# Kernel optimization log

Measured on AMD Instinct MI355X. Metric: run time of the kernel, lower is better.

Reference implementation:

```python
import jax, jax.numpy as jnp
import numpy as np
import math

B, T_FUT, T_LOOK, D, H = 8, 512, 2048, 1024, 16
HD = D // H


def setup_inputs() -> dict:
    key = jax.random.key(0)
    ks = jax.random.split(key, 12)
    xav = 1.0 / math.sqrt(D)  # approx xavier_uniform scale for square [D,D]
    return {
        "encoded_representation": jax.random.normal(ks[0], (B, T_LOOK, D), jnp.float32),
        "future_queries": jax.random.normal(ks[1], (B, T_FUT, D), jnp.float32),
        "decoder_lengths": jax.random.randint(ks[2], (B,), 1, T_FUT + 1),
        "encoder_lengths": jax.random.randint(ks[3], (B,), 1, T_LOOK + 1),
        "wq_w": jax.random.normal(ks[4], (D, D), jnp.float32) * xav,
        "wq_b": jnp.zeros((D,), jnp.float32),
        "wk_w": jax.random.normal(ks[5], (D, D), jnp.float32) * xav,
        "wk_b": jnp.zeros((D,), jnp.float32),
        "wv_w": jax.random.normal(ks[6], (D, D), jnp.float32) * xav,
        "wv_b": jnp.zeros((D,), jnp.float32),
        "wo_w": jax.random.normal(ks[7], (D, D), jnp.float32) * xav,
        "wo_b": jnp.zeros((D,), jnp.float32),
    }


def reference(encoded_representation, future_queries, decoder_lengths, encoder_lengths,
              wq_w, wq_b, wk_w, wk_b, wv_w, wv_b, wo_w, wo_b):
    # variable-length padding mask: [B, 1, T_fut, T_look]
    dec_valid = jnp.arange(T_FUT)[None, :] < decoder_lengths[:, None]   # [B, T_fut]
    enc_valid = jnp.arange(T_LOOK)[None, :] < encoder_lengths[:, None]  # [B, T_look]
    mask = dec_valid[:, None, :, None] & enc_valid[:, None, None, :]

    # torch nn.Linear: y = x @ W^T + b
    Q = (future_queries @ wq_w.T + wq_b).reshape(B, T_FUT, H, HD)
    K = (encoded_representation @ wk_w.T + wk_b).reshape(B, T_LOOK, H, HD)
    V = (encoded_representation @ wv_w.T + wv_b).reshape(B, T_LOOK, H, HD)

    scores = jnp.einsum("bqhd,bkhd->bhqk", Q, K) / math.sqrt(HD)
    # NOTE: faithful to source, which fills masked positions with -1e-09 (not -1e9)
    scores = jnp.where(mask, scores, jnp.float32(-1e-09))
    probs = jax.nn.softmax(scores, axis=-1)

    attended = jnp.einsum("bhqk,bkhd->bqhd", probs, V).reshape(B, T_FUT, D)
    return attended @ wo_w.T + wo_b
```

## Files before the change

kernel.cpp:

```cpp
#include <hip/hip_runtime.h>

typedef __attribute__((ext_vector_type(4))) float f32x4;
typedef __attribute__((ext_vector_type(8))) short s16x8;

__device__ __forceinline__ ushort f2bf(float f) {
  unsigned u = __float_as_uint(f);
  return (ushort)((u + 0x7fffu + ((u >> 16) & 1u)) >> 16);
}

__global__ __launch_bounds__(256) void cvt_bf16(const float4* __restrict__ in,
                                                ushort* __restrict__ out, int n4) {
  int stride = gridDim.x * blockDim.x;
  for (int i = blockIdx.x * blockDim.x + threadIdx.x; i < n4; i += stride) {
    float4 v = in[i];
    uint2 o;
    o.x = (unsigned)f2bf(v.x) | ((unsigned)f2bf(v.y) << 16);
    o.y = (unsigned)f2bf(v.z) | ((unsigned)f2bf(v.w) << 16);
    *(uint2*)(out + (size_t)i * 4) = o;
  }
}

__global__ __launch_bounds__(256) void cvt_bf16_w4(const float4* __restrict__ a,
                                                   const float4* __restrict__ b,
                                                   const float4* __restrict__ c,
                                                   const float4* __restrict__ d,
                                                   ushort* __restrict__ oa, ushort* __restrict__ ob,
                                                   ushort* __restrict__ oc, ushort* __restrict__ od) {
  int idx = blockIdx.x * 256 + threadIdx.x;
  int sel = idx >> 18, k = idx & 262143;
  const float4* src = sel == 0 ? a : sel == 1 ? b : sel == 2 ? c : d;
  ushort* dst = sel == 0 ? oa : sel == 1 ? ob : sel == 2 ? oc : od;
  float4 v = src[k];
  uint2 o;
  o.x = (unsigned)f2bf(v.x) | ((unsigned)f2bf(v.y) << 16);
  o.y = (unsigned)f2bf(v.z) | ((unsigned)f2bf(v.w) << 16);
  *(uint2*)(dst + (size_t)k * 4) = o;
}

__device__ __forceinline__ void gload_lds16(const void* g, void* l) {
  __builtin_amdgcn_global_load_lds((const __attribute__((address_space(1))) void*)g,
                                   (__attribute__((address_space(3))) void*)l, 16, 0, 0);
}

__global__ __launch_bounds__(512, 1) void gemm256_fused(
    const ushort* __restrict__ enc16, const ushort* __restrict__ fq16,
    const ushort* __restrict__ Bkv, const ushort* __restrict__ Bq,
    const float* __restrict__ wk_b, const float* __restrict__ wv_b,
    const float* __restrict__ wq_b,
    ushort* __restrict__ Ko, ushort* __restrict__ Vt, ushort* __restrict__ Qo,
    float* __restrict__ Tsum, const int* __restrict__ dlen,
    const int* __restrict__ elen, float qscale) {
  __shared__ char lds[131072];
  const int tid = threadIdx.x;
  const int lane = tid & 63, wid = tid >> 6;
  const int g = lane >> 4, r = lane & 15;
  const int wm = wid >> 2, wn = wid & 3;
  const int bid = blockIdx.x;

  const ushort* Amat;
  const ushort* Bmat;
  int m0, n0, role;
  if (bid < 512) {
    const int xcd = bid & 7, inner = bid >> 3;
    m0 = (xcd * 8 + (inner & 7)) * 256;
    n0 = (inner >> 3) * 256;
    Amat = enc16;
    Bmat = Bkv;
    if (n0 < 1024) {
      role = 0;
      if ((m0 & 2047) >= elen[m0 >> 11]) return;
    } else {
      role = 1;
    }
  } else {
    const int q = bid - 512;
    m0 = (q & 15) * 256;
    n0 = (q >> 4) * 256;
    Amat = fq16;
    Bmat = Bq;
    role = 2;
    if ((m0 & 511) >= dlen[m0 >> 9]) return;
  }
  const size_t rowb = 2048;

  const int srow = tid >> 3;
  const int scb = (((tid & 7) ^ (srow & 7)) << 4);
  const char* Asrc = (const char*)Amat + (size_t)(m0 + srow) * rowb + scb;
  const char* Bsrc = (const char*)Bmat + (size_t)(n0 + srow) * rowb + scb;

  auto sAh = [&](int kt, int h) {
    char* d0 = lds + (kt & 1) * 32768 + h * 16384 + tid * 16;
    const char* s0 = Asrc + (size_t)(h * 128) * rowb + (size_t)kt * 128;
    gload_lds16(s0, d0);
    gload_lds16(s0 + (size_t)64 * rowb, d0 + 8192);
  };
  auto sBh = [&](int kt, int h) {
    char* d0 = lds + 65536 + (kt & 1) * 32768 + h * 16384 + tid * 16;
    const char* s0 = Bsrc + (size_t)(h * 128) * rowb + (size_t)kt * 128;
    gload_lds16(s0, d0);
    gload_lds16(s0 + (size_t)64 * rowb, d0 + 8192);
  };

  const int cb0 = (g * 16) ^ ((r & 7) << 4);
  const int cb1 = (64 + g * 16) ^ ((r & 7) << 4);

  f32x4 acc[8][4] = {};

  sAh(0, 0); sAh(0, 1); sBh(0, 0); sBh(0, 1); sBh(1, 0); sBh(1, 1);
  asm volatile("s_waitcnt vmcnt(4)" ::: "memory");
  __builtin_amdgcn_s_barrier();

#define MFMA_(a, b, c) __builtin_amdgcn_mfma_f32_16x16x32_bf16(a, b, c, 0, 0, 0)
#define PH(AB, Q, STAGE, WAIT)                                                 \
  {                                                                            \
    s16x8 aq0 = *(const s16x8*)(AB + (2 * (Q)) * 2048 + cb0);                  \
    s16x8 aq1 = *(const s16x8*)(AB + (2 * (Q)) * 2048 + cb1);                  \
    s16x8 aq2 = *(const s16x8*)(AB + (2 * (Q) + 1) * 2048 + cb0);              \
    s16x8 aq3 = *(const s16x8*)(AB + (2 * (Q) + 1) * 2048 + cb1);              \
    STAGE;                                                                     \
    __builtin_amdgcn_s_barrier();                                              \
    asm volatile("s_waitcnt lgkmcnt(0)" ::: "memory");                         \
    __builtin_amdgcn_sched_barrier(0);                                         \
    __builtin_amdgcn_s_setprio(1);                                             \
    _Pragma("unroll") for (int ni = 0; ni < 4; ++ni)                           \
        acc[2 * (Q)][ni] = MFMA_(aq0, bfr[ni][0], acc[2 * (Q)][ni]);           \
    _Pragma("unroll") for (int ni = 0; ni < 4; ++ni)                           \
        acc[2 * (Q) + 1][ni] = MFMA_(aq2, bfr[ni][0], acc[2 * (Q) + 1][ni]);   \
    _Pragma("unroll") for (int ni = 0; ni < 4; ++ni)                           \
        acc[2 * (Q)][ni] = MFMA_(aq1, bfr[ni][1], acc[2 * (Q)][ni]);           \
    _Pragma("unroll") for (int ni = 0; ni < 4; ++ni)                           \
        acc[2 * (Q) + 1][ni] = MFMA_(aq3, bfr[ni][1], acc[2 * (Q) + 1][ni]);   \
    __builtin_amdgcn_s_setprio(0);                                             \
    WAIT;                                                                      \
    __builtin_amdgcn_s_barrier();                                              \
  }
#define LOADB(BB)                                                              \
  _Pragma("unroll") for (int ni = 0; ni < 4; ++ni) {                           \
    bfr[ni][0] = *(const s16x8*)(BB + ni * 2048 + cb0);                        \
    bfr[ni][1] = *(const s16x8*)(BB + ni * 2048 + cb1);                        \
  }

  const int NIT = 8;
  const char* AbB = lds + wm * 16384 + r * 128;
  const char* BbB = lds + 65536 + (wn >> 1) * 16384 + (wn & 1) * 8192 + r * 128;

  for (int it = 0; it < NIT; ++it) {
    const bool st = (it + 1 < NIT);
    const int k1 = 2 * it + 1, k2 = 2 * it + 2, k3 = 2 * it + 3;
    s16x8 bfr[4][2];
    LOADB(BbB);
    PH(AbB, 0, sAh(k1, 0), );
    PH(AbB, 1, sAh(k1, 1), );
    PH(AbB, 2, if (st) sBh(k2, 0), );
    PH(AbB, 3, if (st) sBh(k2, 1),
       if (st) { asm volatile("s_waitcnt vmcnt(4)" ::: "memory"); } else {
         asm volatile("s_waitcnt vmcnt(0)" ::: "memory");
       });
    const char* Ab1 = AbB + 32768;
    const char* Bb1 = BbB + 32768;
    LOADB(Bb1);
    PH(Ab1, 0, if (st) sAh(k2, 0), );
    PH(Ab1, 1, if (st) sAh(k2, 1), );
    PH(Ab1, 2, if (st) sBh(k3, 0), );
    PH(Ab1, 3, if (st) sBh(k3, 1),
       if (st) { asm volatile("s_waitcnt vmcnt(4)" ::: "memory"); });
  }
#undef PH
#undef LOADB
#undef MFMA_

  if (role != 1) {
    ushort* C = (role == 2) ? Qo : Ko;
    const float* bias0 = (role == 2) ? wq_b : wk_b;
    const float sc = (role == 2) ? qscale : 1.0f;
#pragma unroll
    for (int ni = 0; ni < 4; ++ni) {
      const int col = wn * 64 + ni * 16 + r;
      const float bv = bias0[n0 + col];
#pragma unroll
      for (int i = 0; i < 8; ++i)
#pragma unroll
        for (int j = 0; j < 4; ++j) {
          const int row = wm * 128 + i * 16 + g * 4 + j;
          *(ushort*)(lds + ((row * 512 + col * 2) ^ (((row >> 2) & 7) << 4))) =
              f2bf((acc[i][ni][j] + bv) * sc);
        }
    }
    __syncthreads();
    const int c = tid & 31, r0 = tid >> 5;
#pragma unroll
    for (int u = 0; u < 16; ++u) {
      const int row = u * 16 + r0;
      s16x8 v = *(const s16x8*)(lds + ((row * 512 + c * 16) ^ (((row >> 2) & 7) << 4)));
      *(s16x8*)(C + (size_t)(m0 + row) * 1024 + n0 + c * 8) = v;
    }
  } else {
    const int nv0 = n0 - 1024;
    const int bb = m0 >> 11, tt0 = m0 & 2047;
#pragma unroll
    for (int ni = 0; ni < 4; ++ni) {
      const int nv = nv0 + wn * 64 + ni * 16 + r;
      const float bv = wv_b[nv];
#pragma unroll
      for (int qq = 0; qq < 2; ++qq) {
        float s = 0.0f;
#pragma unroll
        for (int ii = 0; ii < 4; ++ii)
#pragma unroll
          for (int j = 0; j < 4; ++j) s += acc[qq * 4 + ii][ni][j];
        s += __shfl_xor(s, 16);
        s += __shfl_xor(s, 32);
        if (g == 0) {
          const int gt = (m0 + (wm * 2 + qq) * 64) >> 6;
          Tsum[((size_t)((gt >> 5) * 16 + (nv >> 6)) * 33 + (gt & 31)) * 64 + (nv & 63)] =
              s + 64.0f * bv;
        }
      }
    }
#pragma unroll
    for (int ni = 0; ni < 4; ++ni) {
      const int rowl = wn * 64 + ni * 16 + r;
      const float bv = wv_b[nv0 + rowl];
#pragma unroll
      for (int i = 0; i < 8; ++i)
#pragma unroll
        for (int j = 0; j < 4; ++j) {
          const int coll = wm * 128 + i * 16 + g * 4 + j;
          *(ushort*)(lds + ((rowl * 512 + coll * 2) ^ ((rowl & 7) << 4))) =
              f2bf(acc[i][ni][j] + bv);
        }
    }
    __syncthreads();
    const int c = tid & 31, r0 = tid >> 5;
#pragma unroll
    for (int u = 0; u < 16; ++u) {
      const int row = u * 16 + r0;
      s16x8 v = *(const s16x8*)(lds + ((row * 512 + c * 16) ^ ((row & 7) << 4)));
      *(s16x8*)(Vt + ((size_t)bb * 1024 + nv0 + row) * 2048 + tt0 + c * 8) = v;
    }
  }
}

template <int EPI>
__global__ __launch_bounds__(256) void gemm_bt(const ushort* __restrict__ A,
                                               const ushort* __restrict__ B,
                                               const float* __restrict__ bias,
                                               void* __restrict__ Cout, float oscale,
                                               int M, int N, int K) {
  __shared__ ushort As[128 * 32];
  __shared__ ushort Bs[128 * 32];
  const int tid = threadIdx.x;
  const int lane = tid & 63, w = tid >> 6;
  const int g = lane >> 4, r = lane & 15;
  const int m0 = blockIdx.x * 128, n0 = blockIdx.y * 128;
  const int wm = (w >> 1) * 64, wn = (w & 1) * 64;

  const int srow = tid >> 2;
  const int scb = (tid & 3) * 16;
  const char* Ag = (const char*)(A + (size_t)(m0 + srow) * K) + scb;
  const char* Bg = (const char*)(B + (size_t)(n0 + srow) * K) + scb;
  char* AsB = (char*)As + (tid & 192) * 16;
  char* BsB = (char*)Bs + (tid & 192) * 16;
  const size_t rowskip = (size_t)64 * K * sizeof(ushort);

  f32x4 acc[4][4] = {};

  for (int k0 = 0; k0 < K; k0 += 32) {
    gload_lds16(Ag + (size_t)k0 * 2, AsB);
    gload_lds16(Ag + rowskip + (size_t)k0 * 2, AsB + 4096);
    gload_lds16(Bg + (size_t)k0 * 2, BsB);
    gload_lds16(Bg + rowskip + (size_t)k0 * 2, BsB + 4096);
    __syncthreads();
    s16x8 af[4], bf[4];
#pragma unroll
    for (int i = 0; i < 4; ++i) af[i] = *(const s16x8*)&As[(wm + i * 16 + r) * 32 + g * 8];
#pragma unroll
    for (int i = 0; i < 4; ++i) bf[i] = *(const s16x8*)&Bs[(wn + i * 16 + r) * 32 + g * 8];
#pragma unroll
    for (int mi = 0; mi < 4; ++mi)
#pragma unroll
      for (int ni = 0; ni < 4; ++ni)
        acc[mi][ni] =
            __builtin_amdgcn_mfma_f32_16x16x32_bf16(af[mi], bf[ni], acc[mi][ni], 0, 0, 0);
    __syncthreads();
  }

  if constexpr (EPI == 0) {
    ushort* C = (ushort*)Cout;
#pragma unroll
    for (int ni = 0; ni < 4; ++ni) {
      const int n = n0 + wn + ni * 16 + r;
      const float bv = bias[n];
#pragma unroll
      for (int mi = 0; mi < 4; ++mi) {
        const int mb = m0 + wm + mi * 16 + g * 4;
#pragma unroll
        for (int j = 0; j < 4; ++j)
          C[(size_t)(mb + j) * N + n] = f2bf((acc[mi][ni][j] + bv) * oscale);
      }
    }
  } else {
    float* C = (float*)Cout;
#pragma unroll
    for (int ni = 0; ni < 4; ++ni) {
      const int n = n0 + wn + ni * 16 + r;
      const float bv = bias[n];
#pragma unroll
      for (int mi = 0; mi < 4; ++mi) {
        const int mb = m0 + wm + mi * 16 + g * 4;
#pragma unroll
        for (int j = 0; j < 4; ++j)
          C[(size_t)(mb + j) * N + n] = acc[mi][ni][j] + bv;
      }
    }
  }
}

__global__ __launch_bounds__(64) void vsuffix(float* __restrict__ T) {
  const int bh = blockIdx.x;
  const int d = threadIdx.x;
  float* p = T + (size_t)bh * 33 * 64 + d;
  float run = 0.0f;
  p[32 * 64] = 0.0f;
  for (int t = 31; t >= 0; --t) {
    run += p[t * 64];
    p[t * 64] = run;
  }
}

__device__ __forceinline__ ushort* swz(ushort* base, int row, int colb) {
  return (ushort*)((char*)base + row * 128 + (colb ^ ((row & 7) << 4)));
}

__global__ __launch_bounds__(256) void attn_fwd(
    const ushort* __restrict__ Q, const ushort* __restrict__ Km,
    const ushort* __restrict__ Vt, const float* __restrict__ Vsuf,
    const int* __restrict__ dlen, const int* __restrict__ elen,
    ushort* __restrict__ Oatt) {
  const int tid = threadIdx.x;
  const int lane = tid & 63, w = tid >> 6;
  const int g = lane >> 4, r = lane & 15;
  const int qt = blockIdx.x, b = blockIdx.y, h = blockIdx.z;
  const int dl = dlen[b], el = elen[b];
  const float* VS = Vsuf + (size_t)(b * 16 + h) * 33 * 64;

  if (qt * 64 >= dl) {
    const int qrow = qt * 64 + w * 16 + g * 4;
#pragma unroll
    for (int dt = 0; dt < 4; ++dt) {
      const ushort hv = f2bf(VS[dt * 16 + r] * (1.0f / 2048.0f));
#pragma unroll
      for (int j = 0; j < 4; ++j)
        Oatt[(size_t)(b * 512 + qrow + j) * 1024 + h * 64 + dt * 16 + r] = hv;
    }
    return;
  }

  __shared__ ushort Ks[64 * 64];
  __shared__ ushort Vs[64 * 64];
  __shared__ ushort Ps[4 * 16 * 64];
  ushort* PsW = Ps + w * 16 * 64;
  const int qbase = qt * 64 + w * 16;

  s16x8 qf[2];
  {
    const ushort* qp = Q + (size_t)(b * 512 + qbase + r) * 1024 + h * 64 + g * 8;
    qf[0] = *(const s16x8*)qp;
    qf[1] = *(const s16x8*)(qp + 32);
  }

  f32x4 o[4] = {};
  float lrow[4] = {0.0f, 0.0f, 0.0f, 0.0f};
  bool qok[4];
#pragma unroll
  for (int j = 0; j < 4; ++j) qok[j] = (qbase + g * 4 + j) < dl;

  const int sr = tid >> 3;
  const int sc8 = (tid & 7) * 8;
  const int scb = sc8 * 2;
  const ushort* Kg = Km + (size_t)(b * 2048 + sr) * 1024 + h * 64 + sc8;
  const ushort* Vg = Vt + ((size_t)b * 1024 + h * 64 + sr) * 2048 + sc8;

  const int t_last = (el - 1) >> 6;

  s16x8 pk0, pk1, pv0, pv1;
  {
    pk0 = *(const s16x8*)(Kg);
    pk1 = *(const s16x8*)(Kg + (size_t)32 * 1024);
    pv0 = *(const s16x8*)(Vg);
    pv1 = *(const s16x8*)(Vg + (size_t)32 * 2048);
  }

  for (int t = 0; t <= t_last; ++t) {
    *(s16x8*)swz(Ks, sr, scb) = pk0;
    *(s16x8*)swz(Ks, sr + 32, scb) = pk1;
    *(s16x8*)swz(Vs, sr, scb) = pv0;
    *(s16x8*)swz(Vs, sr + 32, scb) = pv1;
    __syncthreads();

    if (t < t_last) {
      const int kv0 = (t + 1) * 64;
      pk0 = *(const s16x8*)(Kg + (size_t)kv0 * 1024);
      pk1 = *(const s16x8*)(Kg + (size_t)(kv0 + 32) * 1024);
      pv0 = *(const s16x8*)(Vg + kv0);
      pv1 = *(const s16x8*)(Vg + (size_t)32 * 2048 + kv0);
    }

    const int kv0 = t * 64;
    float p[4][4];
#pragma unroll
    for (int nt = 0; nt < 4; ++nt) {
      f32x4 s = {};
      s16x8 kf0 = *(const s16x8*)swz(Ks, nt * 16 + r, g * 16);
      s16x8 kf1 = *(const s16x8*)swz(Ks, nt * 16 + r, 64 + g * 16);
      s = __builtin_amdgcn_mfma_f32_16x16x32_bf16(qf[0], kf0, s, 0, 0, 0);
      s = __builtin_amdgcn_mfma_f32_16x16x32_bf16(qf[1], kf1, s, 0, 0, 0);
      const bool kok = (kv0 + nt * 16 + r) < el;
#pragma unroll
      for (int j = 0; j < 4; ++j) {
        const float pe = __builtin_amdgcn_exp2f(s[j]);
        p[nt][j] = (kok && qok[j]) ? pe : 1.0f;
      }
    }
#pragma unroll
    for (int nt = 0; nt < 4; ++nt)
#pragma unroll
      for (int j = 0; j < 4; ++j) lrow[j] += p[nt][j];

#pragma unroll
    for (int nt = 0; nt < 4; ++nt) {
#pragma unroll
      for (int jp = 0; jp < 4; jp += 2) {
        unsigned pk;
        asm("v_cvt_pk_bf16_f32 %0, %1, %2" : "=v"(pk) : "v"(p[nt][jp]), "v"(p[nt][jp + 1]));
        *swz(PsW, g * 4 + jp, (nt * 16 + r) * 2) = (ushort)pk;
        *swz(PsW, g * 4 + jp + 1, (nt * 16 + r) * 2) = (ushort)(pk >> 16);
      }
    }

#pragma unroll
    for (int kc = 0; kc < 2; ++kc) {
      s16x8 pf = *(const s16x8*)swz(PsW, r, kc * 64 + g * 16);
#pragma unroll
      for (int dt = 0; dt < 4; ++dt) {
        s16x8 vf = *(const s16x8*)swz(Vs, dt * 16 + r, kc * 64 + g * 16);
        o[dt] = __builtin_amdgcn_mfma_f32_16x16x32_bf16(pf, vf, o[dt], 0, 0, 0);
      }
    }
    __syncthreads();
  }

  const float tailcnt = (float)(2048 - (t_last + 1) * 64);
  const float* VT = VS + (t_last + 1) * 64;
#pragma unroll
  for (int dt = 0; dt < 4; ++dt) {
    const float tv = VT[dt * 16 + r];
#pragma unroll
    for (int j = 0; j < 4; ++j) o[dt][j] += tv;
  }

  float inv[4];
#pragma unroll
  for (int j = 0; j < 4; ++j) {
    float s = lrow[j];
    s += __shfl_xor(s, 1);
    s += __shfl_xor(s, 2);
    s += __shfl_xor(s, 4);
    s += __shfl_xor(s, 8);
    inv[j] = 1.0f / (s + tailcnt);
  }
#pragma unroll
  for (int dt = 0; dt < 4; ++dt)
#pragma unroll
    for (int j = 0; j < 4; ++j)
      Oatt[(size_t)(b * 512 + qbase + g * 4 + j) * 1024 + h * 64 + dt * 16 + r] =
          f2bf(o[dt][j] * inv[j]);
}

extern "C" void kernel_launch(void* const* d_in, const int* in_sizes, int n_in,
                              void* d_out, int out_size, void* d_ws, size_t ws_size,
                              hipStream_t stream) {
  const float* enc  = (const float*)d_in[0];
  const float* fq   = (const float*)d_in[1];
  const int* dlen   = (const int*)d_in[2];
  const int* elen   = (const int*)d_in[3];
  const float* wq_w = (const float*)d_in[4];
  const float* wq_b = (const float*)d_in[5];
  const float* wk_w = (const float*)d_in[6];
  const float* wk_b = (const float*)d_in[7];
  const float* wv_w = (const float*)d_in[8];
  const float* wv_b = (const float*)d_in[9];
  const float* wo_w = (const float*)d_in[10];
  const float* wo_b = (const float*)d_in[11];

  char* ws = (char*)d_ws;
  ushort* enc16 = (ushort*)(ws + 0);
  ushort* fq16  = (ushort*)(ws + 33554432);
  float*  Vsuf  = (float*)(ws + 41943040 + 2097152 * 4);
  ushort* wq16  = (ushort*)(ws + 41943040);
  ushort* wk16  = (ushort*)(ws + 44040192);
  ushort* wv16  = (ushort*)(ws + 46137344);
  ushort* wo16  = (ushort*)(ws + 48234496);
  ushort* Qw    = (ushort*)(ws + 52428800);
  ushort* Kw    = (ushort*)(ws + 60817408);
  ushort* Vtw   = (ushort*)(ws + 94371840);
  ushort* attw  = (ushort*)(ws + 127926272);

  cvt_bf16<<<2048, 256, 0, stream>>>((const float4*)enc, enc16, 16384 * 1024 / 4);
  cvt_bf16<<<1024, 256, 0, stream>>>((const float4*)fq, fq16, 4096 * 1024 / 4);
  cvt_bf16_w4<<<4096, 256, 0, stream>>>((const float4*)wq_w, (const float4*)wk_w,
                                        (const float4*)wv_w, (const float4*)wo_w,
                                        wq16, wk16, wv16, wo16);

  const float qscale = 0.125f * 1.44269504088896340736f;
  gemm256_fused<<<576, 512, 0, stream>>>(enc16, fq16, wk16, wq16, wk_b, wv_b, wq_b,
                                         Kw, Vtw, Qw, Vsuf, dlen, elen, qscale);
  vsuffix<<<128, 64, 0, stream>>>(Vsuf);

  attn_fwd<<<dim3(8, 8, 16), 256, 0, stream>>>(Qw, Kw, Vtw, Vsuf, dlen, elen, attw);

  gemm_bt<2><<<dim3(32, 8), 256, 0, stream>>>(attw, wo16, wo_b, d_out, 1.0f, 4096, 1024, 1024);
}
```

Measured before the change: 198.2 us.

## Make projection GEMM persistent with atomic tile queue and merge conversion kernels

The fused QKV projection GEMM now launches 256 persistent blocks. Each block pulls 256x256 tiles from a global atomic counter, and tiles masked out by the length checks are skipped without occupying a block slot. This is meant to balance load across CUs and avoid the tail effect of a 576-block grid. The three bf16 conversion kernels are merged into one grid-stride kernel, and the attention output buffer now reuses the fq16 workspace region. The changes add a memset launch and an atomic per tile, and drop the XCD-aware tile ordering. There is also a possible race on the shared tile index when a block skips a tile.

Result: slower. 319.1 us (+61.0%).

```diff
diff --git a/kernel.cpp b/kernel.cpp
--- a/kernel.cpp
+++ b/kernel.cpp
@@ -8,33 +8,34 @@
   return (ushort)((u + 0x7fffu + ((u >> 16) & 1u)) >> 16);
 }
 
-__global__ __launch_bounds__(256) void cvt_bf16(const float4* __restrict__ in,
-                                                ushort* __restrict__ out, int n4) {
-  int stride = gridDim.x * blockDim.x;
-  for (int i = blockIdx.x * blockDim.x + threadIdx.x; i < n4; i += stride) {
-    float4 v = in[i];
+__global__ __launch_bounds__(256) void cvt_all(
+    const float4* __restrict__ enc, const float4* __restrict__ fq,
+    const float4* __restrict__ wq, const float4* __restrict__ wk,
+    const float4* __restrict__ wv, const float4* __restrict__ wo,
+    ushort* __restrict__ enc16, ushort* __restrict__ fq16,
+    ushort* __restrict__ wq16, ushort* __restrict__ wk16,
+    ushort* __restrict__ wv16, ushort* __restrict__ wo16) {
+  const int stride = gridDim.x * 256;
+  for (int i = blockIdx.x * 256 + threadIdx.x; i < 6291456; i += stride) {
+    const float4* src;
+    ushort* dst;
+    int k;
+    if (i < 4194304) {
+      src = enc; dst = enc16; k = i;
+    } else if (i < 5242880) {
+      src = fq; dst = fq16; k = i - 4194304;
+    } else {
+      const int j = i - 5242880, sel = j >> 18;
+      k = j & 262143;
+      src = sel == 0 ? wq : sel == 1 ? wk : sel == 2 ? wv : wo;
+      dst = sel == 0 ? wq16 : sel == 1 ? wk16 : sel == 2 ? wv16 : wo16;
+    }
+    float4 v = src[k];
     uint2 o;
     o.x = (unsigned)f2bf(v.x) | ((unsigned)f2bf(v.y) << 16);
     o.y = (unsigned)f2bf(v.z) | ((unsigned)f2bf(v.w) << 16);
-    *(uint2*)(out + (size_t)i * 4) = o;
-  }
-}
-
-__global__ __launch_bounds__(256) void cvt_bf16_w4(const float4* __restrict__ a,
-                                                   const float4* __restrict__ b,
-                                                   const float4* __restrict__ c,
-                                                   const float4* __restrict__ d,
-                                                   ushort* __restrict__ oa, ushort* __restrict__ ob,
-                                                   ushort* __restrict__ oc, ushort* __restrict__ od) {
-  int idx = blockIdx.x * 256 + threadIdx.x;
-  int sel = idx >> 18, k = idx & 262143;
-  const float4* src = sel == 0 ? a : sel == 1 ? b : sel == 2 ? c : d;
-  ushort* dst = sel == 0 ? oa : sel == 1 ? ob : sel == 2 ? oc : od;
-  float4 v = src[k];
-  uint2 o;
-  o.x = (unsigned)f2bf(v.x) | ((unsigned)f2bf(v.y) << 16);
-  o.y = (unsigned)f2bf(v.z) | ((unsigned)f2bf(v.w) << 16);
-  *(uint2*)(dst + (size_t)k * 4) = o;
+    *(uint2*)(dst + (size_t)k * 4) = o;
+  }
 }
 
 __device__ __forceinline__ void gload_lds16(const void* g, void* l) {
@@ -49,66 +50,71 @@
     const float* __restrict__ wq_b,
     ushort* __restrict__ Ko, ushort* __restrict__ Vt, ushort* __restrict__ Qo,
     float* __restrict__ Tsum, const int* __restrict__ dlen,
-    const int* __restrict__ elen, float qscale) {
+    const int* __restrict__ elen, unsigned* __restrict__ ctr, float qscale) {
   __shared__ char lds[131072];
+  __shared__ int s_tile;
   const int tid = threadIdx.x;
   const int lane = tid & 63, wid = tid >> 6;
   const int g = lane >> 4, r = lane & 15;
   const int wm = wid >> 2, wn = wid & 3;
-  const int bid = blockIdx.x;
-
-  const ushort* Amat;
-  const ushort* Bmat;
-  int m0, n0, role;
-  if (bid < 512) {
-    const int xcd = bid & 7, inner = bid >> 3;
-    m0 = (xcd * 8 + (inner & 7)) * 256;
-    n0 = (inner >> 3) * 256;
-    Amat = enc16;
-    Bmat = Bkv;
-    if (n0 < 1024) {
-      role = 0;
-      if ((m0 & 2047) >= elen[m0 >> 11]) return;
+
+  for (;;) {
+    if (tid == 0) s_tile = (int)atomicAdd(ctr, 1u);
+    __syncthreads();
+    const int t = s_tile;
+    if (t >= 576) return;
+
+    const ushort* Amat;
+    const ushort* Bmat;
+    int m0, n0, role;
+    if (t < 512) {
+      m0 = (t & 63) * 256;
+      n0 = (t >> 6) * 256;
+      Amat = enc16;
+      Bmat = Bkv;
+      if (n0 < 1024) {
+        role = 0;
+        if ((m0 & 2047) >= elen[m0 >> 11]) continue;
+      } else {
+        role = 1;
+      }
     } else {
-      role = 1;
-    }
-  } else {
-    const int q = bid - 512;
-    m0 = (q & 15) * 256;
-    n0 = (q >> 4) * 256;
-    Amat = fq16;
-    Bmat = Bq;
-    role = 2;
-    if ((m0 & 511) >= dlen[m0 >> 9]) return;
-  }
-  const size_t rowb = 2048;
-
-  const int srow = tid >> 3;
-  const int scb = (((tid & 7) ^ (srow & 7)) << 4);
-  const char* Asrc = (const char*)Amat + (size_t)(m0 + srow) * rowb + scb;
-  const char* Bsrc = (const char*)Bmat + (size_t)(n0 + srow) * rowb + scb;
-
-  auto sAh = [&](int kt, int h) {
-    char* d0 = lds + (kt & 1) * 32768 + h * 16384 + tid * 16;
-    const char* s0 = Asrc + (size_t)(h * 128) * rowb + (size_t)kt * 128;
-    gload_lds16(s0, d0);
-    gload_lds16(s0 + (size_t)64 * rowb, d0 + 8192);
-  };
-  auto sBh = [&](int kt, int h) {
-    char* d0 = lds + 65536 + (kt & 1) * 32768 + h * 16384 + tid * 16;
-    const char* s0 = Bsrc + (size_t)(h * 128) * rowb + (size_t)kt * 128;
-    gload_lds16(s0, d0);
-    gload_lds16(s0 + (size_t)64 * rowb, d0 + 8192);
-  };
-
-  const int cb0 = (g * 16) ^ ((r & 7) << 4);
-  const int cb1 = (64 + g * 16) ^ ((r & 7) << 4);
-
-  f32x4 acc[8][4] = {};
-
-  sAh(0, 0); sAh(0, 1); sBh(0, 0); sBh(0, 1); sBh(1, 0); sBh(1, 1);
-  asm volatile("s_waitcnt vmcnt(4)" ::: "memory");
-  __builtin_amdgcn_s_barrier();
+      const int q = t - 512;
+      m0 = (q & 15) * 256;
+      n0 = (q >> 4) * 256;
+      Amat = fq16;
+      Bmat = Bq;
+      role = 2;
+      if ((m0 & 511) >= dlen[m0 >> 9]) continue;
+    }
+    const size_t rowb = 2048;
+
+    const int srow = tid >> 3;
+    const int scb = (((tid & 7) ^ (srow & 7)) << 4);
+    const char* Asrc = (const char*)Amat + (size_t)(m0 + srow) * rowb + scb;
+    const char* Bsrc = (const char*)Bmat + (size_t)(n0 + srow) * rowb + scb;
+
+    auto sAh = [&](int kt, int h) {
+      char* d0 = lds + (kt & 1) * 32768 + h * 16384 + tid * 16;
+      const char* s0 = Asrc + (size_t)(h * 128) * rowb + (size_t)kt * 128;
+      gload_lds16(s0, d0);
+      gload_lds16(s0 + (size_t)64 * rowb, d0 + 8192);
+    };
+    auto sBh = [&](int kt, int h) {
+      char* d0 = lds + 65536 + (kt & 1) * 32768 + h * 16384 + tid * 16;
+      const char* s0 = Bsrc + (size_t)(h * 128) * rowb + (size_t)kt * 128;
+      gload_lds16(s0, d0);
+      gload_lds16(s0 + (size_t)64 * rowb, d0 + 8192);
+    };
+
+    const int cb0 = (g * 16) ^ ((r & 7) << 4);
+    const int cb1 = (64 + g * 16) ^ ((r & 7) << 4);
+
+    f32x4 acc[8][4] = {};
+
+    sAh(0, 0); sAh(0, 1); sBh(0, 0); sBh(0, 1); sBh(1, 0); sBh(1, 1);
+    asm volatile("s_waitcnt vmcnt(4)" ::: "memory");
+    __builtin_amdgcn_s_barrier();
 
 #define MFMA_(a, b, c) __builtin_amdgcn_mfma_f32_16x16x32_bf16(a, b, c, 0, 0, 0)
 #define PH(AB, Q, STAGE, WAIT)                                                 \
@@ -140,113 +146,111 @@
     bfr[ni][1] = *(const s16x8*)(BB + ni * 2048 + cb1);                        \
   }
 
-  const int NIT = 8;
-  const char* AbB = lds + wm * 16384 + r * 128;
-  const char* BbB = lds + 65536 + (wn >> 1) * 16384 + (wn & 1) * 8192 + r * 128;
-
-  for (int it = 0; it < NIT; ++it) {
-    const bool st = (it + 1 < NIT);
-    const int k1 = 2 * it + 1, k2 = 2 * it + 2, k3 = 2 * it + 3;
-    s16x8 bfr[4][2];
-    LOADB(BbB);
-    PH(AbB, 0, sAh(k1, 0), );
-    PH(AbB, 1, sAh(k1, 1), );
-    PH(AbB, 2, if (st) sBh(k2, 0), );
-    PH(AbB, 3, if (st) sBh(k2, 1),
-       if (st) { asm volatile("s_waitcnt vmcnt(4)" ::: "memory"); } else {
-         asm volatile("s_waitcnt vmcnt(0)" ::: "memory");
-       });
-    const char* Ab1 = AbB + 32768;
-    const char* Bb1 = BbB + 32768;
-    LOADB(Bb1);
-    PH(Ab1, 0, if (st) sAh(k2, 0), );
-    PH(Ab1, 1, if (st) sAh(k2, 1), );
-    PH(Ab1, 2, if (st) sBh(k3, 0), );
-    PH(Ab1, 3, if (st) sBh(k3, 1),
-       if (st) { asm volatile("s_waitcnt vmcnt(4)" ::: "memory"); });
-  }
+    const char* AbB = lds + wm * 16384 + r * 128;
+    const char* BbB = lds + 65536 + (wn >> 1) * 16384 + (wn & 1) * 8192 + r * 128;
+
+    for (int it = 0; it < 8; ++it) {
+      const bool st = (it + 1 < 8);
+      const int k1 = 2 * it + 1, k2 = 2 * it + 2, k3 = 2 * it + 3;
+      s16x8 bfr[4][2];
+      LOADB(BbB);
+      PH(AbB, 0, sAh(k1, 0), );
+      PH(AbB, 1, sAh(k1, 1), );
+      PH(AbB, 2, if (st) sBh(k2, 0), );
+      PH(AbB, 3, if (st) sBh(k2, 1),
+         if (st) { asm volatile("s_waitcnt vmcnt(4)" ::: "memory"); } else {
+           asm volatile("s_waitcnt vmcnt(0)" ::: "memory");
+         });
+      const char* Ab1 = AbB + 32768;
+      const char* Bb1 = BbB + 32768;
+      LOADB(Bb1);
+      PH(Ab1, 0, if (st) sAh(k2, 0), );
+      PH(Ab1, 1, if (st) sAh(k2, 1), );
+      PH(Ab1, 2, if (st) sBh(k3, 0), );
+      PH(Ab1, 3, if (st) sBh(k3, 1),
+         if (st) { asm volatile("s_waitcnt vmcnt(4)" ::: "memory"); });
+    }
 #undef PH
 #undef LOADB
 #undef MFMA_
 
-  if (role != 1) {
-    ushort* C = (role == 2) ? Qo : Ko;
-    const float* bias0 = (role == 2) ? wq_b : wk_b;
-    const float sc = (role == 2) ? qscale : 1.0f;
-#pragma unroll
-    for (int ni = 0; ni < 4; ++ni) {
-      const int col = wn * 64 + ni * 16 + r;
-      const float bv = bias0[n0 + col];
-#pragma unroll
-      for (int i = 0; i < 8; ++i)
-#pragma unroll
-        for (int j = 0; j < 4; ++j) {
-          const int row = wm * 128 + i * 16 + g * 4 + j;
-          *(ushort*)(lds + ((row * 512 + col * 2) ^ (((row >> 2) & 7) << 4))) =
-              f2bf((acc[i][ni][j] + bv) * sc);
+    if (role != 1) {
+      ushort* C = (role == 2) ? Qo : Ko;
+      const float* bias0 = (role == 2) ? wq_b : wk_b;
+      const float sc = (role == 2) ? qscale : 1.0f;
+#pragma unroll
+      for (int ni = 0; ni < 4; ++ni) {
+        const int col = wn * 64 + ni * 16 + r;
+        const float bv = bias0[n0 + col];
+#pragma unroll
+        for (int i = 0; i < 8; ++i)
+#pragma unroll
+          for (int j = 0; j < 4; ++j) {
+            const int row = wm * 128 + i * 16 + g * 4 + j;
+            *(ushort*)(lds + ((row * 512 + col * 2) ^ (((row >> 2) & 7) << 4))) =
+                f2bf((acc[i][ni][j] + bv) * sc);
+          }
+      }
+      __syncthreads();
+      const int c = tid & 31, r0 = tid >> 5;
+#pragma unroll
+      for (int u = 0; u < 16; ++u) {
+        const int row = u * 16 + r0;
+        s16x8 v = *(const s16x8*)(lds + ((row * 512 + c * 16) ^ (((row >> 2) & 7) << 4)));
+        *(s16x8*)(C + (size_t)(m0 + row) * 1024 + n0 + c * 8) = v;
+      }
+    } else {
+      const int nv0 = n0 - 1024;
+      const int bb = m0 >> 11, tt0 = m0 & 2047;
+#pragma unroll
+      for (int ni = 0; ni < 4; ++ni) {
+        const int nv = nv0 + wn * 64 + ni * 16 + r;
+        const float bv = wv_b[nv];
+#pragma unroll
+        for (int qq = 0; qq < 2; ++qq) {
+          float s = 0.0f;
+#pragma unroll
+          for (int ii = 0; ii < 4; ++ii)
+#pragma unroll
+            for (int j = 0; j < 4; ++j) s += acc[qq * 4 + ii][ni][j];
+          s += __shfl_xor(s, 16);
+          s += __shfl_xor(s, 32);
+          if (g == 0) {
+            const int gt = (m0 + (wm * 2 + qq) * 64) >> 6;
+            Tsum[((size_t)((gt >> 5) * 16 + (nv >> 6)) * 33 + (gt & 31)) * 64 + (nv & 63)] =
+                s + 64.0f * bv;
+          }
         }
-    }
-    __syncthreads();
-    const int c = tid & 31, r0 = tid >> 5;
-#pragma unroll
-    for (int u = 0; u < 16; ++u) {
-      const int row = u * 16 + r0;
-      s16x8 v = *(const s16x8*)(lds + ((row * 512 + c * 16) ^ (((row >> 2) & 7) << 4)));
-      *(s16x8*)(C + (size_t)(m0 + row) * 1024 + n0 + c * 8) = v;
-    }
-  } else {
-    const int nv0 = n0 - 1024;
-    const int bb = m0 >> 11, tt0 = m0 & 2047;
-#pragma unroll
-    for (int ni = 0; ni < 4; ++ni) {
-      const int nv = nv0 + wn * 64 + ni * 16 + r;
-      const float bv = wv_b[nv];
-#pragma unroll
-      for (int qq = 0; qq < 2; ++qq) {
-        float s = 0.0f;
-#pragma unroll
-        for (int ii = 0; ii < 4; ++ii)
-#pragma unroll
-          for (int j = 0; j < 4; ++j) s += acc[qq * 4 + ii][ni][j];
-        s += __shfl_xor(s, 16);
-        s += __shfl_xor(s, 32);
-        if (g == 0) {
-          const int gt = (m0 + (wm * 2 + qq) * 64) >> 6;
-          Tsum[((size_t)((gt >> 5) * 16 + (nv >> 6)) * 33 + (gt & 31)) * 64 + (nv & 63)] =
-              s + 64.0f * bv;
-        }
-      }
-    }
-#pragma unroll
-    for (int ni = 0; ni < 4; ++ni) {
-      const int rowl = wn * 64 + ni * 16 + r;
-      const float bv = wv_b[nv0 + rowl];
-#pragma unroll
-      for (int i = 0; i < 8; ++i)
-#pragma unroll
-        for (int j = 0; j < 4; ++j) {
-          const int coll = wm * 128 + i * 16 + g * 4 + j;
-          *(ushort*)(lds + ((rowl * 512 + coll * 2) ^ ((rowl & 7) << 4))) =
-              f2bf(acc[i][ni][j] + bv);
-        }
-    }
-    __syncthreads();
-    const int c = tid & 31, r0 = tid >> 5;
-#pragma unroll
-    for (int u = 0; u < 16; ++u) {
-      const int row = u * 16 + r0;
-      s16x8 v = *(const s16x8*)(lds + ((row * 512 + c * 16) ^ ((row & 7) << 4)));
-      *(s16x8*)(Vt + ((size_t)bb * 1024 + nv0 + row) * 2048 + tt0 + c * 8) = v;
-    }
-  }
-}
-
-template <int EPI>
-__global__ __launch_bounds__(256) void gemm_bt(const ushort* __restrict__ A,
-                                               const ushort* __restrict__ B,
-                                               const float* __restrict__ bias,
-                                               void* __restrict__ Cout, float oscale,
-                                               int M, int N, int K) {
+      }
+#pragma unroll
+      for (int ni = 0; ni < 4; ++ni) {
+        const int rowl = wn * 64 + ni * 16 + r;
+        const float bv = wv_b[nv0 + rowl];
+#pragma unroll
+        for (int i = 0; i < 8; ++i)
+#pragma unroll
+          for (int j = 0; j < 4; ++j) {
+            const int coll = wm * 128 + i * 16 + g * 4 + j;
+            *(ushort*)(lds + ((rowl * 512 + coll * 2) ^ ((rowl & 7) << 4))) =
+                f2bf(acc[i][ni][j] + bv);
+          }
+      }
+      __syncthreads();
+      const int c = tid & 31, r0 = tid >> 5;
+#pragma unroll
+      for (int u = 0; u < 16; ++u) {
+        const int row = u * 16 + r0;
+        s16x8 v = *(const s16x8*)(lds + ((row * 512 + c * 16) ^ ((row & 7) << 4)));
+        *(s16x8*)(Vt + ((size_t)bb * 1024 + nv0 + row) * 2048 + tt0 + c * 8) = v;
+      }
+    }
+  }
+}
+
+__global__ __launch_bounds__(256) void oproj(const ushort* __restrict__ A,
+                                             const ushort* __restrict__ B,
+                                             const float* __restrict__ bias,
+                                             float* __restrict__ C, int M, int N, int K) {
   __shared__ ushort As[128 * 32];
   __shared__ ushort Bs[128 * 32];
   const int tid = threadIdx.x;
@@ -285,33 +289,16 @@
     __syncthreads();
   }
 
-  if constexpr (EPI == 0) {
-    ushort* C = (ushort*)Cout;
-#pragma unroll
-    for (int ni = 0; ni < 4; ++ni) {
-      const int n = n0 + wn + ni * 16 + r;
-      const float bv = bias[n];
-#pragma unroll
-      for (int mi = 0; mi < 4; ++mi) {
-        const int mb = m0 + wm + mi * 16 + g * 4;
-#pragma unroll
-        for (int j = 0; j < 4; ++j)
-          C[(size_t)(mb + j) * N + n] = f2bf((acc[mi][ni][j] + bv) * oscale);
-      }
-    }
-  } else {
-    float* C = (float*)Cout;
-#pragma unroll
-    for (int ni = 0; ni < 4; ++ni) {
-      const int n = n0 + wn + ni * 16 + r;
-      const float bv = bias[n];
-#pragma unroll
-      for (int mi = 0; mi < 4; ++mi) {
-        const int mb = m0 + wm + mi * 16 + g * 4;
-#pragma unroll
-        for (int j = 0; j < 4; ++j)
-          C[(size_t)(mb + j) * N + n] = acc[mi][ni][j] + bv;
-      }
+#pragma unroll
+  for (int ni = 0; ni < 4; ++ni) {
+    const int n = n0 + wn + ni * 16 + r;
+    const float bv = bias[n];
+#pragma unroll
+    for (int mi = 0; mi < 4; ++mi) {
+      const int mb = m0 + wm + mi * 16 + g * 4;
+#pragma unroll
+      for (int j = 0; j < 4; ++j)
+        C[(size_t)(mb + j) * N + n] = acc[mi][ni][j] + bv;
     }
   }
 }
@@ -496,28 +483,29 @@
   char* ws = (char*)d_ws;
   ushort* enc16 = (ushort*)(ws + 0);
   ushort* fq16  = (ushort*)(ws + 33554432);
-  float*  Vsuf  = (float*)(ws + 41943040 + 2097152 * 4);
+  ushort* attw  = (ushort*)(ws + 33554432);
   ushort* wq16  = (ushort*)(ws + 41943040);
   ushort* wk16  = (ushort*)(ws + 44040192);
   ushort* wv16  = (ushort*)(ws + 46137344);
   ushort* wo16  = (ushort*)(ws + 48234496);
+  float*  Vsuf  = (float*)(ws + 50331648);
+  unsigned* ctr = (unsigned*)(ws + 51904512);
   ushort* Qw    = (ushort*)(ws + 52428800);
   ushort* Kw    = (ushort*)(ws + 60817408);
   ushort* Vtw   = (ushort*)(ws + 94371840);
-  ushort* attw  = (ushort*)(ws + 127926272);
-
-  cvt_bf16<<<2048, 256, 0, stream>>>((const float4*)enc, enc16, 16384 * 1024 / 4);
-  cvt_bf16<<<1024, 256, 0, stream>>>((const float4*)fq, fq16, 4096 * 1024 / 4);
-  cvt_bf16_w4<<<4096, 256, 0, stream>>>((const float4*)wq_w, (const float4*)wk_w,
-                                        (const float4*)wv_w, (const float4*)wo_w,
-                                        wq16, wk16, wv16, wo16);
+
+  hipMemsetAsync(ctr, 0, 4, stream);
+  cvt_all<<<4096, 256, 0, stream>>>((const float4*)enc, (const float4*)fq,
+                                    (const float4*)wq_w, (const float4*)wk_w,
+                                    (const float4*)wv_w, (const float4*)wo_w,
+                                    enc16, fq16, wq16, wk16, wv16, wo16);
 
   const float qscale = 0.125f * 1.44269504088896340736f;
-  gemm256_fused<<<576, 512, 0, stream>>>(enc16, fq16, wk16, wq16, wk_b, wv_b, wq_b,
-                                         Kw, Vtw, Qw, Vsuf, dlen, elen, qscale);
+  gemm256_fused<<<256, 512, 0, stream>>>(enc16, fq16, wk16, wq16, wk_b, wv_b, wq_b,
+                                         Kw, Vtw, Qw, Vsuf, dlen, elen, ctr, qscale);
   vsuffix<<<128, 64, 0, stream>>>(Vsuf);
 
   attn_fwd<<<dim3(8, 8, 16), 256, 0, stream>>>(Qw, Kw, Vtw, Vsuf, dlen, elen, attw);
 
-  gemm_bt<2><<<dim3(32, 8), 256, 0, stream>>>(attw, wo16, wo_b, d_out, 1.0f, 4096, 1024, 1024);
-}
+  oproj<<<dim3(32, 8), 256, 0, stream>>>(attw, wo16, wo_b, (float*)d_out, 4096, 1024, 1024);
+}
```
